# Optimization experiments

Measured on AMD Instinct MI355X. Metric: run time of the kernel, lower is better.

## Reference

```python
import jax, jax.numpy as jnp
import numpy as np

B, N, C, H, W = 32, 32, 3, 32, 32
HID, OUT = 256, 128


def _conv(x, w, b):
    y = jax.lax.conv_general_dilated(
        x, w, window_strides=(1, 1), padding="SAME",
        dimension_numbers=("NCHW", "OIHW", "NCHW"))
    return y + b[None, :, None, None]


def _sage(h, lw, lb, rw):
    # PyG SAGEConv with mean aggregation on a fully-connected graph (no self-loops):
    # agg_i = (sum_j h_j - h_i) / (N-1); out = agg @ lw.T + lb + h @ rw.T
    n = h.shape[1]
    agg = (jnp.sum(h, axis=1, keepdims=True) - h) / (n - 1)
    return jnp.einsum('bnd,od->bno', agg, lw) + lb + jnp.einsum('bnd,od->bno', h, rw)


def setup_inputs() -> dict:
    key = jax.random.key(0)
    ks = jax.random.split(key, 16)
    def g(k, shape, scale):
        return jax.random.normal(k, shape, dtype=jnp.float32) * scale
    return {
        "x": jax.random.normal(ks[0], (B, N, C, H, W), dtype=jnp.float32),
        "mask": jnp.ones((B, N), dtype=jnp.float32),
        "conv1_w": g(ks[1], (64, C, 3, 3), 0.1),
        "conv1_b": jnp.zeros((64,), jnp.float32),
        "conv2_w": g(ks[2], (128, 64, 3, 3), 0.05),
        "conv2_b": jnp.zeros((128,), jnp.float32),
        "fc_w": g(ks[3], (HID, 128), 0.08),
        "fc_b": jnp.zeros((HID,), jnp.float32),
        "s1_lw": g(ks[4], (HID, HID), 0.06),
        "s1_lb": jnp.zeros((HID,), jnp.float32),
        "s1_rw": g(ks[5], (HID, HID), 0.06),
        "s2_lw": g(ks[6], (OUT, HID), 0.06),
        "s2_lb": jnp.zeros((OUT,), jnp.float32),
        "s2_rw": g(ks[7], (OUT, HID), 0.06),
    }


def reference(x, mask, conv1_w, conv1_b, conv2_w, conv2_b, fc_w, fc_b,
              s1_lw, s1_lb, s1_rw, s2_lw, s2_lb, s2_rw):
    b, n, c, h, w = x.shape
    z = x.reshape(b * n, c, h, w)
    z = jax.nn.relu(_conv(z, conv1_w, conv1_b))
    z = jax.nn.relu(_conv(z, conv2_w, conv2_b))
    z = jnp.mean(z, axis=(2, 3))                      # AdaptiveAvgPool2d((1,1)) + flatten
    z = z @ fc_w.T + fc_b                             # [B*N, HID]
    z = z.reshape(b, n, -1) * mask[:, :, None]
    z = jax.nn.relu(_sage(z, s1_lw, s1_lb, s1_rw))
    z = _sage(z, s2_lw, s2_lb, s2_rw)                 # [B, N, OUT]
    return z
```

## Files before the change

kernel.cpp:

```cpp
#include <hip/hip_runtime.h>
#include <hip/hip_bf16.h>


typedef __attribute__((ext_vector_type(8))) short bfrag;
typedef __attribute__((ext_vector_type(4))) float f32x4;
typedef __attribute__((ext_vector_type(16))) float f32x16;

static __device__ __forceinline__ unsigned short f2bf(float f) {
    union { float f; unsigned u; } v; v.f = f;
    unsigned r = v.u + 0x7fff + ((v.u >> 16) & 1);
    return (unsigned short)(r >> 16);
}

__global__ __launch_bounds__(256) void prep_kernel(
    const float* __restrict__ s1lw, const float* __restrict__ s1rw,
    const float* __restrict__ s2lw, const float* __restrict__ s2rw,
    const float* __restrict__ c2w, const float* __restrict__ c1w,
    const float* __restrict__ c1b, const float* __restrict__ fcw,
    float* __restrict__ l1T, float* __restrict__ w1pT,
    float* __restrict__ l2T, float* __restrict__ w2pT,
    float* __restrict__ fwT,
    short* __restrict__ w2c, short* __restrict__ w1b,
    float* __restrict__ pooled) {
    int i = blockIdx.x * 256 + threadIdx.x;
    const float inv31 = 1.f / 31.f;
    if (i < 65536) {
        int d = i >> 8, o = i & 255;
        float lw = s1lw[o * 256 + d];
        l1T[i]  = lw;
        w1pT[i] = s1rw[o * 256 + d] - lw * inv31;
        pooled[i] = 0.f;
        pooled[i + 65536] = 0.f;
    }
    if (i < 32768) {
        int d = i >> 7, o = i & 127;
        float lw = s2lw[o * 256 + d];
        l2T[i]  = lw;
        w2pT[i] = s2rw[o * 256 + d] - lw * inv31;
        int c = i >> 8, o2 = i & 255;
        fwT[i] = fcw[o2 * 128 + c];
    }
    if (i < 73728) {
        int tap = i >> 13, r = i & 8191;
        int ks = r >> 11, hi = (r >> 10) & 1, oc = (r >> 3) & 127, j = i & 7;
        int ic = ks * 16 + hi * 8 + j;
        w2c[i] = (short)f2bf(c2w[(oc * 64 + ic) * 9 + tap]);
    }
    if (i < 2048) {
        int oc = i >> 5, k = i & 31;
        float v = (k < 27) ? c1w[oc * 27 + k] : (k == 27 ? c1b[oc] : 0.f);
        w1b[i] = (short)f2bf(v);
    }
}

__global__ __launch_bounds__(256, 3) void fused_conv_kernel(
    const float* __restrict__ x, const short* __restrict__ w1b,
    const short* __restrict__ w2c, const float* __restrict__ b2,
    float* __restrict__ pooled) {
    const int band = blockIdx.x, img = blockIdx.y;
    __shared__ short xt[3 * 8 * 34];
    __shared__ short c1t[6 * 34 * 72];
    __shared__ float wsum[4][128];
    const int t = threadIdx.x;
    const int w = t >> 6, lane = t & 63;
    const int ln15 = lane & 15, q8 = (lane >> 4) * 8;
    const int ln31 = lane & 31, hi = lane >> 5;

    const float* xi = x + img * 3072;
    for (int idx = t; idx < 816; idx += 256) {
        int c = idx / 272, rem = idx % 272, r = rem / 34, col = rem % 34;
        int y = band * 4 - 2 + r, xx = col - 1;
        float v = 0.f;
        if ((unsigned)y < 32u && (unsigned)xx < 32u) v = xi[c * 1024 + y * 32 + xx];
        xt[idx] = (short)f2bf(v);
    }
    {
        f32x4 z = {0.f, 0.f, 0.f, 0.f};
        for (int i = t; i < 108; i += 256) {
            int r = i / 18, rem = i % 18, side = rem / 9, q = rem % 9;
            *(f32x4*)(c1t + (r * 34 + side * 33) * 72 + q * 8) = z;
        }
    }
    bfrag b1f[4];
#pragma unroll
    for (int ot = 0; ot < 4; ++ot)
        b1f[ot] = *(const bfrag*)(w1b + (ot * 16 + ln15) * 32 + q8);

    int xOff[8]; int kMask[8]; int kOvr[8];
#pragma unroll
    for (int j = 0; j < 8; ++j) {
        int k = q8 + j;
        int c = (k * 57) >> 9;
        int rem = k - 9 * c;
        int dy = (rem * 11) >> 5;
        int dx = rem - 3 * dy;
        int cc = c < 3 ? c : 2;
        xOff[j] = cc * 272 + dy * 34 + dx;
        kMask[j] = (c < 3) ? 0xFFFF : 0;
        kOvr[j]  = (c < 3) ? 0 : (k == 27 ? 0x3F80 : 0);
    }
    __syncthreads();

#pragma unroll 1
    for (int pt = 0; pt < 3; ++pt) {
        const int tile = w * 3 + pt;
        const int posA = tile * 16 + ln15;
        const int baseA = (posA >> 5) * 34 + (posA & 31);
        bfrag a1f;
#pragma unroll
        for (int j = 0; j < 8; ++j)
            a1f[j] = (short)((xt[xOff[j] + baseA] & kMask[j]) | kOvr[j]);
        f32x4 acc1[4];
#pragma unroll
        for (int ot = 0; ot < 4; ++ot) {
#pragma unroll
            for (int rg = 0; rg < 4; ++rg) acc1[ot][rg] = 0.f;
            acc1[ot] = __builtin_amdgcn_mfma_f32_16x16x32_bf16(
                a1f, b1f[ot], acc1[ot], 0, 0, 0);
        }
#pragma unroll
        for (int rg = 0; rg < 4; ++rg) {
            int pos = tile * 16 + (lane >> 4) * 4 + rg;
            int r = pos >> 5, xc = pos & 31;
            int y = band * 4 - 1 + r;
            bool valid = (unsigned)y < 32u;
#pragma unroll
            for (int ot = 0; ot < 4; ++ot) {
                float v = fmaxf(acc1[ot][rg], 0.f);
                c1t[(r * 34 + xc + 1) * 72 + ot * 16 + ln15] =
                    valid ? (short)f2bf(v) : (short)0;
            }
        }
    }
    __syncthreads();

    float b2v[4];
#pragma unroll
    for (int ot = 0; ot < 4; ++ot) b2v[ot] = b2[ot * 32 + ln31];

    f32x16 acc[4];
#pragma unroll
    for (int ot = 0; ot < 4; ++ot)
#pragma unroll
        for (int rg = 0; rg < 16; ++rg) acc[ot][rg] = 0.f;

    const int aB0 = (w * 34 + ln31) * 72 + hi * 8;
    const short* bPtr = w2c + hi * 1024 + ln31 * 8;

    bfrag bX[8], bY[8];
    auto loadB = [&](bfrag* bf, int st) {
        const short* p = bPtr + st * 4096;
#pragma unroll
        for (int kk = 0; kk < 2; ++kk)
#pragma unroll
            for (int ot = 0; ot < 4; ++ot)
                bf[kk * 4 + ot] = *(const bfrag*)(p + kk * 2048 + ot * 256);
    };
    auto computeS = [&](int st, const bfrag* bf) {
        const int tap = st >> 1, kh = st & 1;
        const int dy = (tap * 11) >> 5, dx = tap - 3 * dy;
        const int a0 = aB0 + (dy * 34 + dx) * 72 + kh * 32;
        bfrag af0 = *(const bfrag*)&c1t[a0];
        bfrag af1 = *(const bfrag*)&c1t[a0 + 16];
#pragma unroll
        for (int ot = 0; ot < 4; ++ot)
            acc[ot] = __builtin_amdgcn_mfma_f32_32x32x16_bf16(
                af0, bf[ot], acc[ot], 0, 0, 0);
#pragma unroll
        for (int ot = 0; ot < 4; ++ot)
            acc[ot] = __builtin_amdgcn_mfma_f32_32x32x16_bf16(
                af1, bf[4 + ot], acc[ot], 0, 0, 0);
    };

    loadB(bX, 0);
#pragma unroll 1
    for (int st = 0; st < 18; st += 2) {
        loadB(bY, st + 1);
        computeS(st, bX);
        if (st + 2 < 18) loadB(bX, st + 2);
        computeS(st + 1, bY);
    }

#pragma unroll
    for (int ot = 0; ot < 4; ++ot) {
        float s = 0.f;
#pragma unroll
        for (int rg = 0; rg < 16; ++rg)
            s += fmaxf(acc[ot][rg] + b2v[ot], 0.f);
        s += __shfl_xor(s, 32, 64);
        if (lane < 32) wsum[w][ot * 32 + ln31] = s;
    }
    __syncthreads();
    if (t < 128) {
        atomicAdd(&pooled[(size_t)img * 128 + t],
                  wsum[0][t] + wsum[1][t] + wsum[2][t] + wsum[3][t]);
    }
}

__global__ __launch_bounds__(256) void fc_kernel(
    const float* __restrict__ pooled, const float* __restrict__ fwT,
    const float* __restrict__ fb, const float* __restrict__ mask,
    float* __restrict__ z1) {
    const int g = blockIdx.x;
    __shared__ float m[4][128];
    const int t = threadIdx.x;
    if (t < 128) {
#pragma unroll
        for (int i = 0; i < 4; ++i)
            m[i][t] = pooled[(size_t)(g * 4 + i) * 128 + t] * (1.f / 1024.f);
    }
    __syncthreads();
    float a0 = fb[t], a1 = a0, a2 = a0, a3 = a0;
#pragma unroll 4
    for (int c = 0; c < 128; ++c) {
        float wv = fwT[c * 256 + t];
        a0 = fmaf(m[0][c], wv, a0);
        a1 = fmaf(m[1][c], wv, a1);
        a2 = fmaf(m[2][c], wv, a2);
        a3 = fmaf(m[3][c], wv, a3);
    }
    z1[(g * 4 + 0) * 256 + t] = a0 * mask[g * 4 + 0];
    z1[(g * 4 + 1) * 256 + t] = a1 * mask[g * 4 + 1];
    z1[(g * 4 + 2) * 256 + t] = a2 * mask[g * 4 + 2];
    z1[(g * 4 + 3) * 256 + t] = a3 * mask[g * 4 + 3];
}

__global__ __launch_bounds__(256) void sage1_kernel(
    const float* __restrict__ z1, const float* __restrict__ l1T,
    const float* __restrict__ lb, const float* __restrict__ w1pT,
    float* __restrict__ z2) {
    const int bb = blockIdx.x >> 3, chunk = blockIdx.x & 7;
    __shared__ float h[32 * 256];
    __shared__ float sl[256];
    const int t = threadIdx.x;
    const float* zb = z1 + bb * 8192;
    for (int idx = t; idx < 8192; idx += 256) h[idx] = zb[idx];
    __syncthreads();
    float s = 0.f;
#pragma unroll
    for (int n = 0; n < 32; ++n) s += h[n * 256 + t];
    sl[t] = s * (1.f / 31.f);
    __syncthreads();
    float c = lb[t];
#pragma unroll 4
    for (int d = 0; d < 256; ++d) c = fmaf(sl[d], l1T[d * 256 + t], c);
    float acc[4];
#pragma unroll
    for (int i = 0; i < 4; ++i) acc[i] = c;
    for (int d0 = 0; d0 < 256; d0 += 4) {
        float wv0 = w1pT[(d0 + 0) * 256 + t];
        float wv1 = w1pT[(d0 + 1) * 256 + t];
        float wv2 = w1pT[(d0 + 2) * 256 + t];
        float wv3 = w1pT[(d0 + 3) * 256 + t];
#pragma unroll
        for (int i = 0; i < 4; ++i) {
            f32x4 hv = *(const f32x4*)&h[(chunk * 4 + i) * 256 + d0];
            acc[i] = fmaf(hv[0], wv0, acc[i]);
            acc[i] = fmaf(hv[1], wv1, acc[i]);
            acc[i] = fmaf(hv[2], wv2, acc[i]);
            acc[i] = fmaf(hv[3], wv3, acc[i]);
        }
    }
    for (int i = 0; i < 4; ++i)
        z2[(bb * 32 + chunk * 4 + i) * 256 + t] = fmaxf(acc[i], 0.f);
}

__global__ __launch_bounds__(256) void sage2_kernel(
    const float* __restrict__ z2, const float* __restrict__ l2T,
    const float* __restrict__ lb, const float* __restrict__ w2pT,
    float* __restrict__ out) {
    const int bb = blockIdx.x >> 3, chunk = blockIdx.x & 7;
    __shared__ float h[32 * 256];
    __shared__ float sl[256];
    const int t = threadIdx.x;
    const float* zb = z2 + bb * 8192;
    for (int idx = t; idx < 8192; idx += 256) h[idx] = zb[idx];
    __syncthreads();
    float s = 0.f;
#pragma unroll
    for (int n = 0; n < 32; ++n) s += h[n * 256 + t];
    sl[t] = s * (1.f / 31.f);
    __syncthreads();
    const int o = t & 127, half = t >> 7;
    float c = lb[o];
#pragma unroll 4
    for (int d = 0; d < 256; ++d) c = fmaf(sl[d], l2T[d * 128 + o], c);
    float acc[2];
    acc[0] = c; acc[1] = c;
    const int n0 = chunk * 4 + half * 2;
    for (int d0 = 0; d0 < 256; d0 += 4) {
        float wv0 = w2pT[(d0 + 0) * 128 + o];
        float wv1 = w2pT[(d0 + 1) * 128 + o];
        float wv2 = w2pT[(d0 + 2) * 128 + o];
        float wv3 = w2pT[(d0 + 3) * 128 + o];
#pragma unroll
        for (int ii = 0; ii < 2; ++ii) {
            f32x4 hv = *(const f32x4*)&h[(n0 + ii) * 256 + d0];
            acc[ii] = fmaf(hv[0], wv0, acc[ii]);
            acc[ii] = fmaf(hv[1], wv1, acc[ii]);
            acc[ii] = fmaf(hv[2], wv2, acc[ii]);
            acc[ii] = fmaf(hv[3], wv3, acc[ii]);
        }
    }
    for (int ii = 0; ii < 2; ++ii)
        out[(size_t)(bb * 32 + n0 + ii) * 128 + o] = acc[ii];
}

extern "C" void kernel_launch(void* const* d_in, const int* in_sizes, int n_in,
                              void* d_out, int out_size, void* d_ws, size_t ws_size,
                              hipStream_t stream) {
    const float* x    = (const float*)d_in[0];
    const float* mask = (const float*)d_in[1];
    const float* c1w  = (const float*)d_in[2];
    const float* c1b  = (const float*)d_in[3];
    const float* c2w  = (const float*)d_in[4];
    const float* c2b  = (const float*)d_in[5];
    const float* fcw  = (const float*)d_in[6];
    const float* fcb  = (const float*)d_in[7];
    const float* s1lw = (const float*)d_in[8];
    const float* s1lb = (const float*)d_in[9];
    const float* s1rw = (const float*)d_in[10];
    const float* s2lw = (const float*)d_in[11];
    const float* s2lb = (const float*)d_in[12];
    const float* s2rw = (const float*)d_in[13];
    float* out = (float*)d_out;

    char* ws = (char*)d_ws;
    float* pooled  = (float*)(ws);
    float* z1      = (float*)(ws + 2048u * 1024);
    float* z2      = (float*)(ws + 3072u * 1024);
    float* l1T     = (float*)(ws + 4096u * 1024);
    float* w1pT    = (float*)(ws + 4352u * 1024);
    float* l2T     = (float*)(ws + 4608u * 1024);
    float* w2pT    = (float*)(ws + 4736u * 1024);
    float* fwT     = (float*)(ws + 4864u * 1024);
    short* w2c     = (short*)(ws + 4992u * 1024);
    short* w1b     = (short*)(ws + 5136u * 1024);

    prep_kernel<<<dim3(288), 256, 0, stream>>>(s1lw, s1rw, s2lw, s2rw, c2w, c1w, c1b,
                                               fcw, l1T, w1pT, l2T, w2pT, fwT, w2c, w1b,
                                               pooled);
    fused_conv_kernel<<<dim3(8, 1024), 256, 0, stream>>>(x, w1b, w2c, c2b, pooled);
    fc_kernel<<<dim3(256), 256, 0, stream>>>(pooled, fwT, fcb, mask, z1);
    sage1_kernel<<<dim3(256), 256, 0, stream>>>(z1, l1T, s1lb, w1pT, z2);
    sage2_kernel<<<dim3(256), 256, 0, stream>>>(z2, l2T, s2lb, w2pT, out);
}
```

Baseline: 313.1 us.

## Enlarge conv tiles to 16-row halves with 4x register-blocked MFMA and packed conv1 layout

Each block now handles 16 output rows (half an image) instead of 4, so every wave accumulates 4 row groups × 4 output-channel tiles. This reuses each loaded conv2 weight fragment across four times as many MFMAs and cuts halo recomputation of conv1. The conv1 LDS layout changes to channel-chunked 8-wide slices written with packed bf16 conversion and transposed MFMA operands. MFMA sections run at raised priority. The cost is many more accumulator registers, occupancy of 1, and a grid of only 2048 blocks.

```diff
diff --git a/kernel.cpp b/kernel.cpp
--- a/kernel.cpp
+++ b/kernel.cpp
@@ -10,6 +10,12 @@
     union { float f; unsigned u; } v; v.f = f;
     unsigned r = v.u + 0x7fff + ((v.u >> 16) & 1);
     return (unsigned short)(r >> 16);
+}
+
+static __device__ __forceinline__ unsigned cvtpk(float lo, float hi) {
+    unsigned r;
+    asm("v_cvt_pk_bf16_f32 %0, %1, %2" : "=v"(r) : "v"(lo), "v"(hi));
+    return r;
 }
 
 __global__ __launch_bounds__(256) void prep_kernel(
@@ -53,33 +59,30 @@
     }
 }
 
-__global__ __launch_bounds__(256, 3) void fused_conv_kernel(
+__global__ __launch_bounds__(256, 1) void fused_conv_kernel(
     const float* __restrict__ x, const short* __restrict__ w1b,
     const short* __restrict__ w2c, const float* __restrict__ b2,
     float* __restrict__ pooled) {
-    const int band = blockIdx.x, img = blockIdx.y;
-    __shared__ short xt[3 * 8 * 34];
-    __shared__ short c1t[6 * 34 * 72];
+    const int half = blockIdx.x, img = blockIdx.y;
+    __shared__ short xt[3 * 20 * 34];
+    __shared__ short c1t[8 * 18 * 34 * 8];
     __shared__ float wsum[4][128];
     const int t = threadIdx.x;
     const int w = t >> 6, lane = t & 63;
-    const int ln15 = lane & 15, q8 = (lane >> 4) * 8;
+    const int ln15 = lane & 15, q8 = (lane >> 4) * 8, q = lane >> 4;
     const int ln31 = lane & 31, hi = lane >> 5;
 
     const float* xi = x + img * 3072;
-    for (int idx = t; idx < 816; idx += 256) {
-        int c = idx / 272, rem = idx % 272, r = rem / 34, col = rem % 34;
-        int y = band * 4 - 2 + r, xx = col - 1;
+    for (int idx = t; idx < 2040; idx += 256) {
+        int c = idx / 680, rem = idx % 680, xr = rem / 34, col = rem % 34;
+        int y = half * 16 - 2 + xr, xx = col - 1;
         float v = 0.f;
         if ((unsigned)y < 32u && (unsigned)xx < 32u) v = xi[c * 1024 + y * 32 + xx];
         xt[idx] = (short)f2bf(v);
     }
-    {
-        f32x4 z = {0.f, 0.f, 0.f, 0.f};
-        for (int i = t; i < 108; i += 256) {
-            int r = i / 18, rem = i % 18, side = rem / 9, q = rem % 9;
-            *(f32x4*)(c1t + (r * 34 + side * 33) * 72 + q * 8) = z;
-        }
+    for (int i = t; i < 288; i += 256) {
+        int ichi = i / 36, rem = i % 36, s = rem >> 1, side = rem & 1;
+        *(uint4*)&c1t[ichi * 4896 + s * 272 + side * 33 * 8] = uint4{0u, 0u, 0u, 0u};
     }
     bfrag b1f[4];
 #pragma unroll
@@ -95,17 +98,17 @@
         int dy = (rem * 11) >> 5;
         int dx = rem - 3 * dy;
         int cc = c < 3 ? c : 2;
-        xOff[j] = cc * 272 + dy * 34 + dx;
+        xOff[j] = cc * 680 + dy * 34 + dx;
         kMask[j] = (c < 3) ? 0xFFFF : 0;
         kOvr[j]  = (c < 3) ? 0 : (k == 27 ? 0x3F80 : 0);
     }
     __syncthreads();
 
 #pragma unroll 1
-    for (int pt = 0; pt < 3; ++pt) {
-        const int tile = w * 3 + pt;
-        const int posA = tile * 16 + ln15;
-        const int baseA = (posA >> 5) * 34 + (posA & 31);
+    for (int pt = 0; pt < 9; ++pt) {
+        const int tile = w * 9 + pt;
+        const int s = tile >> 1, cb = (tile & 1) << 4;
+        const int baseA = s * 34 + cb + ln15;
         bfrag a1f;
 #pragma unroll
         for (int j = 0; j < 8; ++j)
@@ -116,20 +119,19 @@
 #pragma unroll
             for (int rg = 0; rg < 4; ++rg) acc1[ot][rg] = 0.f;
             acc1[ot] = __builtin_amdgcn_mfma_f32_16x16x32_bf16(
-                a1f, b1f[ot], acc1[ot], 0, 0, 0);
+                b1f[ot], a1f, acc1[ot], 0, 0, 0);
         }
-#pragma unroll
-        for (int rg = 0; rg < 4; ++rg) {
-            int pos = tile * 16 + (lane >> 4) * 4 + rg;
-            int r = pos >> 5, xc = pos & 31;
-            int y = band * 4 - 1 + r;
-            bool valid = (unsigned)y < 32u;
-#pragma unroll
-            for (int ot = 0; ot < 4; ++ot) {
-                float v = fmaxf(acc1[ot][rg], 0.f);
-                c1t[(r * 34 + xc + 1) * 72 + ot * 16 + ln15] =
-                    valid ? (short)f2bf(v) : (short)0;
+        const int imgrow = half * 16 - 1 + s;
+        const bool valid = (unsigned)imgrow < 32u;
+        const int wbase = s * 272 + (cb + ln15 + 1) * 8 + (q & 1) * 4;
+#pragma unroll
+        for (int ot = 0; ot < 4; ++ot) {
+            uint2 pk = {0u, 0u};
+            if (valid) {
+                pk.x = cvtpk(fmaxf(acc1[ot][0], 0.f), fmaxf(acc1[ot][1], 0.f));
+                pk.y = cvtpk(fmaxf(acc1[ot][2], 0.f), fmaxf(acc1[ot][3], 0.f));
             }
+            *(uint2*)&c1t[(2 * ot + (q >> 1)) * 4896 + wbase] = pk;
         }
     }
     __syncthreads();
@@ -138,55 +140,64 @@
 #pragma unroll
     for (int ot = 0; ot < 4; ++ot) b2v[ot] = b2[ot * 32 + ln31];
 
-    f32x16 acc[4];
-#pragma unroll
-    for (int ot = 0; ot < 4; ++ot)
-#pragma unroll
-        for (int rg = 0; rg < 16; ++rg) acc[ot][rg] = 0.f;
-
-    const int aB0 = (w * 34 + ln31) * 72 + hi * 8;
-    const short* bPtr = w2c + hi * 1024 + ln31 * 8;
+    f32x16 acc[4][4];
+#pragma unroll
+    for (int rp = 0; rp < 4; ++rp)
+#pragma unroll
+        for (int ot = 0; ot < 4; ++ot)
+#pragma unroll
+            for (int rg = 0; rg < 16; ++rg) acc[rp][ot][rg] = 0.f;
+
+    const int afBase = hi * 4896 + (w * 4) * 272 + ln31 * 8;
+    const short* bBase = w2c + hi * 1024 + ln31 * 8;
 
     bfrag bX[8], bY[8];
     auto loadB = [&](bfrag* bf, int st) {
-        const short* p = bPtr + st * 4096;
+        const short* p = bBase + (st >> 1) * 8192 + (st & 1) * 4096;
 #pragma unroll
         for (int kk = 0; kk < 2; ++kk)
 #pragma unroll
             for (int ot = 0; ot < 4; ++ot)
                 bf[kk * 4 + ot] = *(const bfrag*)(p + kk * 2048 + ot * 256);
     };
-    auto computeS = [&](int st, const bfrag* bf) {
+    auto body = [&](int st, const bfrag* bc, bfrag* bn) {
+        if (st + 1 < 18) loadB(bn, st + 1);
         const int tap = st >> 1, kh = st & 1;
         const int dy = (tap * 11) >> 5, dx = tap - 3 * dy;
-        const int a0 = aB0 + (dy * 34 + dx) * 72 + kh * 32;
-        bfrag af0 = *(const bfrag*)&c1t[a0];
-        bfrag af1 = *(const bfrag*)&c1t[a0 + 16];
-#pragma unroll
-        for (int ot = 0; ot < 4; ++ot)
-            acc[ot] = __builtin_amdgcn_mfma_f32_32x32x16_bf16(
-                af0, bf[ot], acc[ot], 0, 0, 0);
-#pragma unroll
-        for (int ot = 0; ot < 4; ++ot)
-            acc[ot] = __builtin_amdgcn_mfma_f32_32x32x16_bf16(
-                af1, bf[4 + ot], acc[ot], 0, 0, 0);
+        const int a0 = afBase + kh * 19584 + dy * 272 + dx * 8;
+        bfrag af[8];
+#pragma unroll
+        for (int rp = 0; rp < 4; ++rp)
+#pragma unroll
+            for (int kk = 0; kk < 2; ++kk)
+                af[rp * 2 + kk] = *(const bfrag*)&c1t[a0 + rp * 272 + kk * 9792];
+        __builtin_amdgcn_s_setprio(1);
+#pragma unroll
+        for (int kk = 0; kk < 2; ++kk)
+#pragma unroll
+            for (int rp = 0; rp < 4; ++rp)
+#pragma unroll
+                for (int ot = 0; ot < 4; ++ot)
+                    acc[rp][ot] = __builtin_amdgcn_mfma_f32_32x32x16_bf16(
+                        af[rp * 2 + kk], bc[kk * 4 + ot], acc[rp][ot], 0, 0, 0);
+        __builtin_amdgcn_s_setprio(0);
     };
 
     loadB(bX, 0);
 #pragma unroll 1
     for (int st = 0; st < 18; st += 2) {
-        loadB(bY, st + 1);
-        computeS(st, bX);
-        if (st + 2 < 18) loadB(bX, st + 2);
-        computeS(st + 1, bY);
+        body(st, bX, bY);
+        body(st + 1, bY, bX);
     }
 
 #pragma unroll
     for (int ot = 0; ot < 4; ++ot) {
         float s = 0.f;
 #pragma unroll
-        for (int rg = 0; rg < 16; ++rg)
-            s += fmaxf(acc[ot][rg] + b2v[ot], 0.f);
+        for (int rp = 0; rp < 4; ++rp)
+#pragma unroll
+            for (int rg = 0; rg < 16; ++rg)
+                s += fmaxf(acc[rp][ot][rg] + b2v[ot], 0.f);
         s += __shfl_xor(s, 32, 64);
         if (lane < 32) wsum[w][ot * 32 + ln31] = s;
     }
@@ -340,7 +351,7 @@
     prep_kernel<<<dim3(288), 256, 0, stream>>>(s1lw, s1rw, s2lw, s2rw, c2w, c1w, c1b,
                                                fcw, l1T, w1pT, l2T, w2pT, fwT, w2c, w1b,
                                                pooled);
-    fused_conv_kernel<<<dim3(8, 1024), 256, 0, stream>>>(x, w1b, w2c, c2b, pooled);
+    fused_conv_kernel<<<dim3(2, 1024), 256, 0, stream>>>(x, w1b, w2c, c2b, pooled);
     fc_kernel<<<dim3(256), 256, 0, stream>>>(pooled, fwT, fcb, mask, z1);
     sage1_kernel<<<dim3(256), 256, 0, stream>>>(z1, l1T, s1lb, w1pT, z2);
     sage2_kernel<<<dim3(256), 256, 0, stream>>>(z2, l2T, s2lb, w2pT, out);
```

New measurement: 438.9 us. +40.2%, slower.
